# Kernel optimization log

Measured on AMD Instinct MI355X. Metric: run time of the kernel, lower is better.

The kernel has to match this reference:

```python
import jax, jax.numpy as jnp
import numpy as np


def _dconv(x, W, b, d):
    # dilated 3x3 conv, padding=d so spatial size is preserved (NCHW / OIHW)
    y = jax.lax.conv_general_dilated(
        x, W, window_strides=(1, 1), padding=((d, d), (d, d)),
        rhs_dilation=(d, d), dimension_numbers=('NCHW', 'OIHW', 'NCHW'))
    return y + b[None, :, None, None]


def setup_inputs() -> dict:
    key = jax.random.key(0)
    ks = jax.random.split(key, 12)
    B, C, H, W = 2, 512, 64, 64
    s = 0.02  # keep pre-softmax energies in a sane range
    inp = {
        'x':  jax.random.normal(ks[0], (B, C, H, W), jnp.float32),
        'W1': jax.random.normal(ks[1], (128, 512, 3, 3), jnp.float32) * s,
        'b1': jnp.zeros((128,), jnp.float32),
        'W2': jax.random.normal(ks[2], (128, 512, 3, 3), jnp.float32) * s,
        'b2': jnp.zeros((128,), jnp.float32),
        'W3': jax.random.normal(ks[3], (128, 512, 3, 3), jnp.float32) * s,
        'b3': jnp.zeros((128,), jnp.float32),
        'W4': jax.random.normal(ks[4], (128, 512, 3, 3), jnp.float32) * s,
        'b4': jnp.zeros((128,), jnp.float32),
        'Wd':  jax.random.normal(ks[5], (512, 128), jnp.float32) * s,   # dense, 1x1 no bias
        'Wcc': jax.random.normal(ks[6], (256, 512), jnp.float32) * s,   # CCIFL conv 512->256
        'bcc': jnp.zeros((256,), jnp.float32),
        'Wd2': jax.random.normal(ks[7], (512, 256), jnp.float32) * s,   # dense2, 1x1 no bias
    }
    return inp


def reference(x, W1, b1, W2, b2, W3, b3, W4, b4, Wd, Wcc, bcc, Wd2):
    B, C, H, W = x.shape
    N = H * W
    # four dilated-conv feature maps, flattened to [B, 128, N]
    a1 = jax.nn.relu(_dconv(x, W1, b1, 2)).reshape(B, 128, N)
    a2 = jax.nn.relu(_dconv(x, W2, b2, 3)).reshape(B, 128, N)
    a3 = jax.nn.relu(_dconv(x, W3, b3, 5)).reshape(B, 128, N)
    a4 = jax.nn.relu(_dconv(x, W4, b4, 7)).reshape(B, 128, N)

    # spatial attention 1: softmax(a1^T a2), applied as a4 @ att
    att12 = jax.nn.softmax(jnp.einsum('bcn,bcm->bnm', a1, a2), axis=-1)
    o1 = jnp.einsum('bcn,bnm->bcm', a4, att12).reshape(B, 128, H, W)
    o1 = jnp.einsum('oc,bchw->bohw', Wd, o1)  # dense 128->512

    # spatial attention 2: softmax(a3^T a4), applied as a2 @ att
    att34 = jax.nn.softmax(jnp.einsum('bcn,bcm->bnm', a3, a4), axis=-1)
    o2 = jnp.einsum('bcn,bnm->bcm', a2, att34).reshape(B, 128, H, W)
    o2 = jnp.einsum('oc,bchw->bohw', Wd, o2)

    def ccifl(y):
        # GAP -> 1x1 conv (512->256) -> scalar qk attention (softmax over a 1x1 -> 1)
        g = jnp.mean(y, axis=(2, 3))                        # [B, 512]
        z = jnp.einsum('oc,bc->bo', Wcc, g) + bcc           # [B, 256]
        e = jnp.einsum('bc,bc->b', z, z)[:, None, None]     # [B, 1, 1]
        att = jax.nn.softmax(e, axis=-1)                    # == 1
        return z * att[:, 0, :]                             # [B, 256]

    c1 = jnp.einsum('oc,bc->bo', Wd2, ccifl(o1))            # [B, 512]
    c2 = jnp.einsum('oc,bc->bo', Wd2, ccifl(o2))
    # broadcast [B,512,1,1] channel attention over spatial dims + residual
    return c1[:, :, None, None] + c2[:, :, None, None] + x
```

## Files before the change

kernel.cpp:

```cpp
#include <hip/hip_runtime.h>
#include <hip/hip_bf16.h>

typedef short short8 __attribute__((ext_vector_type(8)));
typedef float f32x4 __attribute__((ext_vector_type(4)));
typedef unsigned short u16;

#define XT_OFF   0
#define XT_BYTES (2*78*78*512*2)
#define WR2_OFF  (XT_OFF + XT_BYTES)
#define WR2_BYTES (2*9*16*8*64*16)
#define AFTER_W  (WR2_OFF + WR2_BYTES)
#define P_OFF    AFTER_W
#define P_BYTES  (4*4*4096*128*2)
#define GA_OFF_P (P_OFF + P_BYTES)
#define CA_OFF   AFTER_W
#define CA_BYTES (4*4096*128*4)
#define GA_OFF_A (CA_OFF + CA_BYTES)
#define GA_BYTES 2048
#define GV_REL   GA_BYTES
#define ZV_REL   (GV_REL + 4*512*4)
#define CV_REL   (ZV_REL + 4*256*4)
#define TAIL_END (CV_REL + 2*512*4)
#define WS_NEED_P ((size_t)GA_OFF_P + TAIL_END)
#define WS_NEED_A ((size_t)GA_OFF_A + TAIL_END)

static __device__ __forceinline__ void async_cp16(u16* lds, const u16* g) {
  __builtin_amdgcn_global_load_lds(
      (const __attribute__((address_space(1))) void*)g,
      (__attribute__((address_space(3))) void*)lds, 16, 0, 0);
}

__global__ void zero_u4(uint4* __restrict__ p, int n) {
  int i = blockIdx.x * blockDim.x + threadIdx.x;
  int st = gridDim.x * blockDim.x;
  uint4 z = {0u, 0u, 0u, 0u};
  for (; i < n; i += st) p[i] = z;
}

__global__ void prep_all(const float* __restrict__ x, u16* __restrict__ xT,
                         const float* __restrict__ W2, const float* __restrict__ W4,
                         u16* __restrict__ Wr2, float* __restrict__ gapacc) {
  int bid = blockIdx.x;
  int t = threadIdx.x;
  if (bid < 1024) {
    __shared__ float tile[64][65];
    int bh = bid >> 3, cc = bid & 7;
    int b = bh >> 6, h = bh & 63;
    int w = t & 63, cq4 = t >> 6;
    int pi = t >> 2, q = t & 3;
#pragma unroll
    for (int i = 0; i < 16; ++i) {
      int ci = cq4 + i * 4;
      tile[ci][w] = x[((b * 512 + cc * 64 + ci) * 4096) + h * 64 + w];
    }
    __syncthreads();
    union { u16 u[16]; uint4 v[2]; } pk;
#pragma unroll
    for (int k = 0; k < 16; ++k) {
      __hip_bfloat16 hb = __float2bfloat16(tile[q * 16 + k][pi]);
      pk.u[k] = *(u16*)&hb;
    }
    u16* dst = xT + ((size_t)(b * 78 + h + 7) * 78 + (pi + 7)) * 512 + cc * 64 + q * 16;
    *(uint4*)dst = pk.v[0];
    *(uint4*)(dst + 8) = pk.v[1];
  } else if (bid < 1312) {
    int hb = bid - 1024;
    size_t off; int cnt;
    if (hb < 256) {
      int b = hb >> 7, rem = hb & 127, h = rem >> 1, side = rem & 1;
      off = ((size_t)(b * 78 + 7 + h) * 78 + (side ? 71 : 0)) * 512;
      cnt = 7 * 512;
    } else {
      int k = hb - 256;
      int b = k >> 4, topbot = (k >> 3) & 1, ch = k & 7;
      off = ((size_t)b * 78 + (topbot ? 71 : 0)) * 78 * 512 + (size_t)ch * 34944;
      cnt = 34944;
    }
    uint4* p = (uint4*)(xT + off);
    int n = cnt >> 3;
    uint4 z = {0u, 0u, 0u, 0u};
    for (int i = t; i < n; i += blockDim.x) p[i] = z;
  } else if (bid < 1568) {
    int idx = bid - 1312;
    int conv = idx >> 7, o = idx & 127;
    const float* W = conv ? W4 : W2;
    __shared__ float sw[4608];
    const float* src = W + (size_t)o * 4608;
    for (int k = 0; k < 18; ++k) sw[t + k * 256] = src[t + k * 256];
    __syncthreads();
    if (t < 144) {
      int tap = t >> 4, kc = t & 15;
      int wn = o >> 6, ni = (o >> 4) & 3;
      size_t base = (size_t)conv * 589824 + (size_t)(tap * 16 + kc) * 4096
                    + (wn * 4 + ni) * 512;
#pragma unroll
      for (int cg = 0; cg < 4; ++cg) {
        union { u16 h[8]; uint4 v; } pk;
#pragma unroll
        for (int e = 0; e < 8; ++e) {
          __hip_bfloat16 hb = __float2bfloat16(sw[(kc * 32 + cg * 8 + e) * 9 + tap]);
          pk.h[e] = *(u16*)&hb;
        }
        int lane = cg * 16 + (o & 15);
        *(uint4*)(Wr2 + base + lane * 8) = pk.v;
      }
    }
  } else {
    gapacc[t] = 0.f;
    gapacc[t + 256] = 0.f;
  }
}

template<int MODE>
__global__ __launch_bounds__(256, 2) void conv_mfma(
    const u16* __restrict__ xT, const u16* __restrict__ Wr2,
    u16* __restrict__ Pp, float* __restrict__ convacc) {
  __shared__ __align__(16) u16 Ab[2][8192];
  int bid = blockIdx.x;
  int xcd = bid & 7, j = bid >> 3, g = j >> 2, cq = j & 3;
  int u = g >> 2, pt = (g & 3) * 8 + xcd;
  int b = u & 1, conv = u >> 1;
  int d = conv ? 7 : 3;
  int h0 = pt * 2;
  const u16* xb = xT + (size_t)b * (78 * 78 * 512);
  int t = threadIdx.x, l = t & 63, wv = t >> 6;
  int wm = wv >> 1, wn = wv & 1;

  int slog = (l & 7) ^ (l >> 3);
  int wq = wv * 8 + (l >> 3);
  const u16* gA[4];
#pragma unroll
  for (int m = 0; m < 4; ++m) {
    int hh = m >> 1, mh = m & 1;
    gA[m] = xb + ((size_t)(h0 + hh - d + 7) * 78 + (mh * 32 + wq - d + 7)) * 512
            + cq * 128 + slog * 8;
  }
  const char* bB = (const char*)Wr2 + (size_t)conv * 1179648
                   + cq * 32768 + wn * 4096 + l * 16;

  int rbase = (wm * 64 + (l & 15)) * 64;
  int rs0 = (((l >> 4)) ^ (l & 7)) * 8;
  int rs1 = ((4 + (l >> 4)) ^ (l & 7)) * 8;

  f32x4 acc[4][4];
#pragma unroll
  for (int i = 0; i < 4; ++i)
#pragma unroll
    for (int jj = 0; jj < 4; ++jj) acc[i][jj] = (f32x4){0.f, 0.f, 0.f, 0.f};

  short8 bf0[2][4], bf1[2][4];

  auto issueA = [&](int buf) {
#pragma unroll
    for (int m = 0; m < 4; ++m)
      async_cp16(&Ab[buf][m * 2048 + wv * 512], gA[m]);
    __builtin_amdgcn_sched_barrier(0);
  };
  auto loadB = [&](short8 bf[2][4]) {
#pragma unroll
    for (int c01 = 0; c01 < 2; ++c01)
#pragma unroll
      for (int ni = 0; ni < 4; ++ni)
        bf[c01][ni] = *(const short8*)(bB + c01 * 8192 + ni * 1024);
  };
  auto cbar = [&]() {
    __builtin_amdgcn_sched_barrier(0);
    asm volatile("s_waitcnt vmcnt(8)" ::: "memory");
    __builtin_amdgcn_s_barrier();
    __builtin_amdgcn_sched_barrier(0);
  };
  auto advance = [&](int s) {
    int dA, dB;
    if (!(s & 1)) { dA = 64; dB = 16384; }
    else {
      dB = 114688;
      int tap = (s + 1) >> 1;
      dA = (tap % 3) ? (512 * d - 64) : (38912 * d - 64);
    }
#pragma unroll
    for (int m = 0; m < 4; ++m) gA[m] += dA;
    bB += dB;
  };
  auto compute = [&](int buf, short8 bf[2][4]) {
    const u16* A = Ab[buf];
    short8 af[2][4];
#pragma unroll
    for (int mi = 0; mi < 4; ++mi) {
      af[0][mi] = *(const short8*)&A[rbase + mi * 1024 + rs0];
      af[1][mi] = *(const short8*)&A[rbase + mi * 1024 + rs1];
    }
#pragma unroll
    for (int c01 = 0; c01 < 2; ++c01)
#pragma unroll
      for (int mi = 0; mi < 4; ++mi)
#pragma unroll
        for (int ni = 0; ni < 4; ++ni)
          acc[mi][ni] = __builtin_amdgcn_mfma_f32_16x16x32_bf16(
              af[c01][mi], bf[c01][ni], acc[mi][ni], 0, 0, 0);
  };

  issueA(0); loadB(bf0); advance(0);
  cbar();
  for (int it = 0; it < 9; ++it) {
    int s = it * 2;
    issueA(1); loadB(bf1); advance(s + 1);
    compute(0, bf0);
    cbar();
    if (it < 8) { issueA(0); loadB(bf0); advance(s + 2); }
    compute(1, bf1);
    cbar();
  }

  if (MODE == 0) {
    u16* PP = Pp + ((size_t)(cq * 4 + u) * 4096 + pt * 128 + wm * 64 + (l >> 4) * 4) * 128
              + wn * 64 + (l & 15);
#pragma unroll
    for (int mi = 0; mi < 4; ++mi)
#pragma unroll
      for (int ni = 0; ni < 4; ++ni)
#pragma unroll
        for (int jj = 0; jj < 4; ++jj) {
          __hip_bfloat16 hv = __float2bfloat16(acc[mi][ni][jj]);
          PP[(mi * 16 + jj) * 128 + ni * 16] = *(u16*)&hv;
        }
  } else {
    float* ca = convacc + (size_t)u * 4096 * 128;
#pragma unroll
    for (int mi = 0; mi < 4; ++mi)
#pragma unroll
      for (int ni = 0; ni < 4; ++ni)
#pragma unroll
        for (int jj = 0; jj < 4; ++jj) {
          int pos = pt * 128 + wm * 64 + mi * 16 + (l >> 4) * 4 + jj;
          int oc = wn * 64 + ni * 16 + (l & 15);
          atomicAdd(&ca[pos * 128 + oc], acc[mi][ni][jj]);
        }
  }
}

__global__ void reduce_gap_p(const u16* __restrict__ P,
                             const float* __restrict__ b2, const float* __restrict__ b4,
                             float* __restrict__ gapacc) {
  int u = blockIdx.x >> 6, g = blockIdx.x & 63;
  int conv = u >> 1;
  const float* bias = conv ? b4 : b2;
  int t = threadIdx.x;
  int oct = (t & 15) * 8, pl = t >> 4;
  float bi[8];
  *(float4*)&bi[0] = *(const float4*)&bias[oct];
  *(float4*)&bi[4] = *(const float4*)&bias[oct + 4];
  float s[8];
#pragma unroll
  for (int e = 0; e < 8; ++e) s[e] = 0.f;
  for (int i = 0; i < 4; ++i) {
    int pos = g * 64 + pl * 4 + i;
    size_t base = ((size_t)u * 4096 + pos) * 128 + oct;
    float v[8];
#pragma unroll
    for (int e = 0; e < 8; ++e) v[e] = bi[e];
#pragma unroll
    for (int cq = 0; cq < 4; ++cq) {
      uint4 q = *(const uint4*)&P[base + (size_t)cq * 2097152];
      unsigned w[4] = {q.x, q.y, q.z, q.w};
#pragma unroll
      for (int k = 0; k < 4; ++k) {
        v[k * 2]     += __builtin_bit_cast(float, (w[k] & 0xffffu) << 16);
        v[k * 2 + 1] += __builtin_bit_cast(float, w[k] & 0xffff0000u);
      }
    }
#pragma unroll
    for (int e = 0; e < 8; ++e) s[e] += v[e] > 0.f ? v[e] : 0.f;
  }
  __shared__ float red[16][128];
#pragma unroll
  for (int e = 0; e < 8; ++e) red[pl][oct + e] = s[e];
  __syncthreads();
  if (t < 128) {
    float acc = 0.f;
#pragma unroll
    for (int r = 0; r < 16; ++r) acc += red[r][t];
    atomicAdd(&gapacc[u * 128 + t], acc);
  }
}

__global__ void reduce_gap_a(const float* __restrict__ convacc,
                             const float* __restrict__ b2, const float* __restrict__ b4,
                             float* __restrict__ gapacc) {
  int unit = blockIdx.x >> 5, chunk = blockIdx.x & 31;
  int conv = unit >> 1;
  const float* bias = conv ? b4 : b2;
  int t = threadIdx.x, oc = t & 127, half = t >> 7;
  const float* ca = convacc + (size_t)unit * 4096 * 128;
  float bi = bias[oc];
  float s = 0.f;
  for (int i = 0; i < 64; ++i) {
    int pos = chunk * 128 + half * 64 + i;
    float v = ca[pos * 128 + oc] + bi;
    s += v > 0.f ? v : 0.f;
  }
  __shared__ float red[2][128];
  red[half][oc] = s;
  __syncthreads();
  if (t < 128) atomicAdd(&gapacc[unit * 128 + t], red[0][t] + red[1][t]);
}

__global__ void dense1(const float* __restrict__ gapacc, const float* __restrict__ Wd,
                       float* __restrict__ gv) {
  int o = blockIdx.x, t = threadIdx.x;
  float w = Wd[o * 128 + t];
  float p0 = w * gapacc[2 * 128 + t];
  float p1 = w * gapacc[0 * 128 + t];
  float p2 = w * gapacc[3 * 128 + t];
  float p3 = w * gapacc[1 * 128 + t];
#pragma unroll
  for (int m = 1; m < 64; m <<= 1) {
    p0 += __shfl_xor(p0, m); p1 += __shfl_xor(p1, m);
    p2 += __shfl_xor(p2, m); p3 += __shfl_xor(p3, m);
  }
  __shared__ float red[2][4];
  if ((t & 63) == 0) {
    red[t >> 6][0] = p0; red[t >> 6][1] = p1;
    red[t >> 6][2] = p2; red[t >> 6][3] = p3;
  }
  __syncthreads();
  if (t < 4) {
    const float inv = 1.f / 4096.f;
    gv[t * 512 + o] = (red[0][t] + red[1][t]) * inv;
  }
}

__global__ void dense2(const float* __restrict__ gv, const float* __restrict__ Wcc,
                       const float* __restrict__ bcc, float* __restrict__ zv) {
  int o = blockIdx.x, t = threadIdx.x;
  float w0 = Wcc[o * 512 + t], w1 = Wcc[o * 512 + 256 + t];
  float p[4];
#pragma unroll
  for (int c = 0; c < 4; ++c)
    p[c] = w0 * gv[c * 512 + t] + w1 * gv[c * 512 + 256 + t];
#pragma unroll
  for (int m = 1; m < 64; m <<= 1)
#pragma unroll
    for (int c = 0; c < 4; ++c) p[c] += __shfl_xor(p[c], m);
  __shared__ float red[4][4];
  if ((t & 63) == 0)
#pragma unroll
    for (int c = 0; c < 4; ++c) red[t >> 6][c] = p[c];
  __syncthreads();
  if (t < 4) {
    float s = bcc[o];
#pragma unroll
    for (int wv = 0; wv < 4; ++wv) s += red[wv][t];
    zv[t * 256 + o] = s;
  }
}

__global__ void dense3(const float* __restrict__ zv, const float* __restrict__ Wd2,
                       float* __restrict__ cvec) {
  int o = blockIdx.x, t = threadIdx.x;
  float w = Wd2[o * 256 + t];
  float p0 = w * (zv[0 * 256 + t] + zv[1 * 256 + t]);
  float p1 = w * (zv[2 * 256 + t] + zv[3 * 256 + t]);
#pragma unroll
  for (int m = 1; m < 64; m <<= 1) {
    p0 += __shfl_xor(p0, m);
    p1 += __shfl_xor(p1, m);
  }
  __shared__ float red[4][2];
  if ((t & 63) == 0) { red[t >> 6][0] = p0; red[t >> 6][1] = p1; }
  __syncthreads();
  if (t < 2) {
    float s = red[0][t] + red[1][t] + red[2][t] + red[3][t];
    cvec[t * 512 + o] = s;
  }
}

__global__ void final_add(const float* __restrict__ x, const float* __restrict__ cvec,
                          float* __restrict__ out) {
  int i = blockIdx.x * blockDim.x + threadIdx.x;
  int st = gridDim.x * blockDim.x;
  const float4* x4 = (const float4*)x;
  float4* o4 = (float4*)out;
  for (; i < 1048576; i += st) {
    int flat = i << 2;
    int b = flat >> 21;
    int ch = (flat >> 12) & 511;
    float c = cvec[b * 512 + ch];
    float4 v = x4[i];
    v.x += c; v.y += c; v.z += c; v.w += c;
    o4[i] = v;
  }
}

extern "C" void kernel_launch(void* const* d_in, const int* in_sizes, int n_in,
                              void* d_out, int out_size, void* d_ws, size_t ws_size,
                              hipStream_t stream) {
  const float* x   = (const float*)d_in[0];
  const float* W2  = (const float*)d_in[3];
  const float* b2  = (const float*)d_in[4];
  const float* W4  = (const float*)d_in[7];
  const float* b4  = (const float*)d_in[8];
  const float* Wd  = (const float*)d_in[9];
  const float* Wcc = (const float*)d_in[10];
  const float* bcc = (const float*)d_in[11];
  const float* Wd2 = (const float*)d_in[12];
  float* out = (float*)d_out;

  char* ws = (char*)d_ws;
  u16* xT  = (u16*)(ws + XT_OFF);
  u16* Wr2 = (u16*)(ws + WR2_OFF);

  const bool partial = ws_size >= WS_NEED_P;
  size_t ga_off = partial ? GA_OFF_P : GA_OFF_A;
  float* gapacc = (float*)(ws + ga_off);
  float* gv     = (float*)(ws + ga_off + GV_REL);
  float* zv     = (float*)(ws + ga_off + ZV_REL);
  float* cvec   = (float*)(ws + ga_off + CV_REL);

  prep_all<<<1569, 256, 0, stream>>>(x, xT, W2, W4, Wr2, gapacc);

  if (partial) {
    u16* Pp = (u16*)(ws + P_OFF);
    conv_mfma<0><<<512, 256, 0, stream>>>(xT, Wr2, Pp, nullptr);
    reduce_gap_p<<<256, 256, 0, stream>>>(Pp, b2, b4, gapacc);
  } else {
    float* convacc = (float*)(ws + CA_OFF);
    zero_u4<<<512, 256, 0, stream>>>((uint4*)convacc, CA_BYTES / 16);
    conv_mfma<1><<<512, 256, 0, stream>>>(xT, Wr2, nullptr, convacc);
    reduce_gap_a<<<128, 256, 0, stream>>>(convacc, b2, b4, gapacc);
  }

  dense1<<<512, 128, 0, stream>>>(gapacc, Wd, gv);
  dense2<<<256, 256, 0, stream>>>(gv, Wcc, bcc, zv);
  dense3<<<512, 256, 0, stream>>>(zv, Wd2, cvec);
  final_add<<<2048, 256, 0, stream>>>(x, cvec, out);
}
```

Before: 56.42 us.

## Fold Wcc·Wd into fused weight, merge dense tail into final add, retile conv waves

Precomputes a fused Wcc·Wd matrix inside the prep kernel so the GAP-to-z path needs one small GEMV instead of two. The Wd2 matvec is folded into final_add, with each block recomputing its channel scalar, which removes two kernel launches. The conv MFMA kernel's wave tiling changes from a 2x2 split to each wave covering all 128 rows and 32 output channels, with fewer B registers and a tighter vmcnt wait. In exchange, final_add blocks repeat a 256-wide dot product and the conv waves read more A fragments from LDS.

```diff
diff --git a/kernel.cpp b/kernel.cpp
--- a/kernel.cpp
+++ b/kernel.cpp
@@ -17,10 +17,9 @@
 #define CA_BYTES (4*4096*128*4)
 #define GA_OFF_A (CA_OFF + CA_BYTES)
 #define GA_BYTES 2048
-#define GV_REL   GA_BYTES
-#define ZV_REL   (GV_REL + 4*512*4)
-#define CV_REL   (ZV_REL + 4*256*4)
-#define TAIL_END (CV_REL + 2*512*4)
+#define ZV_REL   GA_BYTES
+#define WF_REL   (ZV_REL + 4*256*4)
+#define TAIL_END (WF_REL + 256*128*4)
 #define WS_NEED_P ((size_t)GA_OFF_P + TAIL_END)
 #define WS_NEED_A ((size_t)GA_OFF_A + TAIL_END)
 
@@ -39,12 +38,32 @@
 
 __global__ void prep_all(const float* __restrict__ x, u16* __restrict__ xT,
                          const float* __restrict__ W2, const float* __restrict__ W4,
-                         u16* __restrict__ Wr2, float* __restrict__ gapacc) {
+                         const float* __restrict__ Wd, const float* __restrict__ Wcc,
+                         u16* __restrict__ Wr2, float* __restrict__ Wfuse,
+                         float* __restrict__ gapacc) {
+  __shared__ float smem[4608];
   int bid = blockIdx.x;
   int t = threadIdx.x;
-  if (bid < 1024) {
-    __shared__ float tile[64][65];
-    int bh = bid >> 3, cc = bid & 7;
+  if (bid < 256) {
+    int o2 = bid;
+    float* wcc_s = smem;
+    float* part  = smem + 512;
+    wcc_s[t] = Wcc[o2 * 512 + t];
+    wcc_s[t + 256] = Wcc[o2 * 512 + 256 + t];
+    __syncthreads();
+    int c = t & 127, half = t >> 7;
+    float s = 0.f;
+    int o0 = half * 256;
+#pragma unroll 4
+    for (int o = 0; o < 256; ++o)
+      s += wcc_s[o0 + o] * Wd[(o0 + o) * 128 + c];
+    if (half) part[c] = s;
+    __syncthreads();
+    if (!half) Wfuse[o2 * 128 + c] = s + part[c];
+  } else if (bid < 1280) {
+    float (*tile)[65] = (float(*)[65])smem;
+    int pb = bid - 256;
+    int bh = pb >> 3, cc = pb & 7;
     int b = bh >> 6, h = bh & 63;
     int w = t & 63, cq4 = t >> 6;
     int pi = t >> 2, q = t & 3;
@@ -63,8 +82,8 @@
     u16* dst = xT + ((size_t)(b * 78 + h + 7) * 78 + (pi + 7)) * 512 + cc * 64 + q * 16;
     *(uint4*)dst = pk.v[0];
     *(uint4*)(dst + 8) = pk.v[1];
-  } else if (bid < 1312) {
-    int hb = bid - 1024;
+  } else if (bid < 1568) {
+    int hb = bid - 1280;
     size_t off; int cnt;
     if (hb < 256) {
       int b = hb >> 7, rem = hb & 127, h = rem >> 1, side = rem & 1;
@@ -80,11 +99,11 @@
     int n = cnt >> 3;
     uint4 z = {0u, 0u, 0u, 0u};
     for (int i = t; i < n; i += blockDim.x) p[i] = z;
-  } else if (bid < 1568) {
-    int idx = bid - 1312;
+  } else if (bid < 1824) {
+    int idx = bid - 1568;
     int conv = idx >> 7, o = idx & 127;
     const float* W = conv ? W4 : W2;
-    __shared__ float sw[4608];
+    float* sw = smem;
     const float* src = W + (size_t)o * 4608;
     for (int k = 0; k < 18; ++k) sw[t + k * 256] = src[t + k * 256];
     __syncthreads();
@@ -124,7 +143,6 @@
   int h0 = pt * 2;
   const u16* xb = xT + (size_t)b * (78 * 78 * 512);
   int t = threadIdx.x, l = t & 63, wv = t >> 6;
-  int wm = wv >> 1, wn = wv & 1;
 
   int slog = (l & 7) ^ (l >> 3);
   int wq = wv * 8 + (l >> 3);
@@ -136,19 +154,19 @@
             + cq * 128 + slog * 8;
   }
   const char* bB = (const char*)Wr2 + (size_t)conv * 1179648
-                   + cq * 32768 + wn * 4096 + l * 16;
-
-  int rbase = (wm * 64 + (l & 15)) * 64;
+                   + cq * 32768 + wv * 2048 + l * 16;
+
+  int rbase = (l & 15) * 64;
   int rs0 = (((l >> 4)) ^ (l & 7)) * 8;
   int rs1 = ((4 + (l >> 4)) ^ (l & 7)) * 8;
 
-  f32x4 acc[4][4];
-#pragma unroll
-  for (int i = 0; i < 4; ++i)
-#pragma unroll
-    for (int jj = 0; jj < 4; ++jj) acc[i][jj] = (f32x4){0.f, 0.f, 0.f, 0.f};
-
-  short8 bf0[2][4], bf1[2][4];
+  f32x4 acc[8][2];
+#pragma unroll
+  for (int i = 0; i < 8; ++i)
+#pragma unroll
+    for (int jj = 0; jj < 2; ++jj) acc[i][jj] = (f32x4){0.f, 0.f, 0.f, 0.f};
+
+  short8 bf0[2][2], bf1[2][2];
 
   auto issueA = [&](int buf) {
 #pragma unroll
@@ -156,16 +174,16 @@
       async_cp16(&Ab[buf][m * 2048 + wv * 512], gA[m]);
     __builtin_amdgcn_sched_barrier(0);
   };
-  auto loadB = [&](short8 bf[2][4]) {
+  auto loadB = [&](short8 bf[2][2]) {
 #pragma unroll
     for (int c01 = 0; c01 < 2; ++c01)
 #pragma unroll
-      for (int ni = 0; ni < 4; ++ni)
+      for (int ni = 0; ni < 2; ++ni)
         bf[c01][ni] = *(const short8*)(bB + c01 * 8192 + ni * 1024);
   };
   auto cbar = [&]() {
     __builtin_amdgcn_sched_barrier(0);
-    asm volatile("s_waitcnt vmcnt(8)" ::: "memory");
+    asm volatile("s_waitcnt vmcnt(4)" ::: "memory");
     __builtin_amdgcn_s_barrier();
     __builtin_amdgcn_sched_barrier(0);
   };
@@ -181,22 +199,17 @@
     for (int m = 0; m < 4; ++m) gA[m] += dA;
     bB += dB;
   };
-  auto compute = [&](int buf, short8 bf[2][4]) {
+  auto compute = [&](int buf, short8 bf[2][2]) {
     const u16* A = Ab[buf];
-    short8 af[2][4];
-#pragma unroll
-    for (int mi = 0; mi < 4; ++mi) {
-      af[0][mi] = *(const short8*)&A[rbase + mi * 1024 + rs0];
-      af[1][mi] = *(const short8*)&A[rbase + mi * 1024 + rs1];
-    }
-#pragma unroll
-    for (int c01 = 0; c01 < 2; ++c01)
-#pragma unroll
-      for (int mi = 0; mi < 4; ++mi)
-#pragma unroll
-        for (int ni = 0; ni < 4; ++ni)
-          acc[mi][ni] = __builtin_amdgcn_mfma_f32_16x16x32_bf16(
-              af[c01][mi], bf[c01][ni], acc[mi][ni], 0, 0, 0);
+#pragma unroll
+    for (int mi = 0; mi < 8; ++mi) {
+      short8 a0 = *(const short8*)&A[rbase + mi * 1024 + rs0];
+      short8 a1 = *(const short8*)&A[rbase + mi * 1024 + rs1];
+      acc[mi][0] = __builtin_amdgcn_mfma_f32_16x16x32_bf16(a0, bf[0][0], acc[mi][0], 0, 0, 0);
+      acc[mi][1] = __builtin_amdgcn_mfma_f32_16x16x32_bf16(a0, bf[0][1], acc[mi][1], 0, 0, 0);
+      acc[mi][0] = __builtin_amdgcn_mfma_f32_16x16x32_bf16(a1, bf[1][0], acc[mi][0], 0, 0, 0);
+      acc[mi][1] = __builtin_amdgcn_mfma_f32_16x16x32_bf16(a1, bf[1][1], acc[mi][1], 0, 0, 0);
+    }
   };
 
   issueA(0); loadB(bf0); advance(0);
@@ -212,12 +225,12 @@
   }
 
   if (MODE == 0) {
-    u16* PP = Pp + ((size_t)(cq * 4 + u) * 4096 + pt * 128 + wm * 64 + (l >> 4) * 4) * 128
-              + wn * 64 + (l & 15);
-#pragma unroll
-    for (int mi = 0; mi < 4; ++mi)
-#pragma unroll
-      for (int ni = 0; ni < 4; ++ni)
+    u16* PP = Pp + ((size_t)(cq * 4 + u) * 4096 + pt * 128 + (l >> 4) * 4) * 128
+              + wv * 32 + (l & 15);
+#pragma unroll
+    for (int mi = 0; mi < 8; ++mi)
+#pragma unroll
+      for (int ni = 0; ni < 2; ++ni)
 #pragma unroll
         for (int jj = 0; jj < 4; ++jj) {
           __hip_bfloat16 hv = __float2bfloat16(acc[mi][ni][jj]);
@@ -226,13 +239,13 @@
   } else {
     float* ca = convacc + (size_t)u * 4096 * 128;
 #pragma unroll
-    for (int mi = 0; mi < 4; ++mi)
-#pragma unroll
-      for (int ni = 0; ni < 4; ++ni)
+    for (int mi = 0; mi < 8; ++mi)
+#pragma unroll
+      for (int ni = 0; ni < 2; ++ni)
 #pragma unroll
         for (int jj = 0; jj < 4; ++jj) {
-          int pos = pt * 128 + wm * 64 + mi * 16 + (l >> 4) * 4 + jj;
-          int oc = wn * 64 + ni * 16 + (l & 15);
+          int pos = pt * 128 + mi * 16 + (l >> 4) * 4 + jj;
+          int oc = wv * 32 + ni * 16 + (l & 15);
           atomicAdd(&ca[pos * 128 + oc], acc[mi][ni][jj]);
         }
   }
@@ -304,10 +317,10 @@
   if (t < 128) atomicAdd(&gapacc[unit * 128 + t], red[0][t] + red[1][t]);
 }
 
-__global__ void dense1(const float* __restrict__ gapacc, const float* __restrict__ Wd,
-                       float* __restrict__ gv) {
-  int o = blockIdx.x, t = threadIdx.x;
-  float w = Wd[o * 128 + t];
+__global__ void dense_a(const float* __restrict__ gapacc, const float* __restrict__ Wfuse,
+                        const float* __restrict__ bcc, float* __restrict__ zv) {
+  int o2 = blockIdx.x, t = threadIdx.x;
+  float w = Wfuse[o2 * 128 + t];
   float p0 = w * gapacc[2 * 128 + t];
   float p1 = w * gapacc[0 * 128 + t];
   float p2 = w * gapacc[3 * 128 + t];
@@ -325,70 +338,39 @@
   __syncthreads();
   if (t < 4) {
     const float inv = 1.f / 4096.f;
-    gv[t * 512 + o] = (red[0][t] + red[1][t]) * inv;
-  }
-}
-
-__global__ void dense2(const float* __restrict__ gv, const float* __restrict__ Wcc,
-                       const float* __restrict__ bcc, float* __restrict__ zv) {
-  int o = blockIdx.x, t = threadIdx.x;
-  float w0 = Wcc[o * 512 + t], w1 = Wcc[o * 512 + 256 + t];
-  float p[4];
-#pragma unroll
-  for (int c = 0; c < 4; ++c)
-    p[c] = w0 * gv[c * 512 + t] + w1 * gv[c * 512 + 256 + t];
-#pragma unroll
-  for (int m = 1; m < 64; m <<= 1)
-#pragma unroll
-    for (int c = 0; c < 4; ++c) p[c] += __shfl_xor(p[c], m);
-  __shared__ float red[4][4];
-  if ((t & 63) == 0)
-#pragma unroll
-    for (int c = 0; c < 4; ++c) red[t >> 6][c] = p[c];
-  __syncthreads();
-  if (t < 4) {
-    float s = bcc[o];
-#pragma unroll
-    for (int wv = 0; wv < 4; ++wv) s += red[wv][t];
-    zv[t * 256 + o] = s;
-  }
-}
-
-__global__ void dense3(const float* __restrict__ zv, const float* __restrict__ Wd2,
-                       float* __restrict__ cvec) {
-  int o = blockIdx.x, t = threadIdx.x;
-  float w = Wd2[o * 256 + t];
-  float p0 = w * (zv[0 * 256 + t] + zv[1 * 256 + t]);
-  float p1 = w * (zv[2 * 256 + t] + zv[3 * 256 + t]);
+    zv[t * 256 + o2] = bcc[o2] + (red[0][t] + red[1][t]) * inv;
+  }
+}
+
+__global__ void final_add(const float* __restrict__ x, const float* __restrict__ zv,
+                          const float* __restrict__ Wd2, float* __restrict__ out) {
+  int t = threadIdx.x, bid = blockIdx.x;
+  int ch = (bid >> 2) & 511;
+  float w = Wd2[ch * 256 + t];
+  float p0 = w * (zv[t] + zv[256 + t]);
+  float p1 = w * (zv[512 + t] + zv[768 + t]);
 #pragma unroll
   for (int m = 1; m < 64; m <<= 1) {
     p0 += __shfl_xor(p0, m);
     p1 += __shfl_xor(p1, m);
   }
   __shared__ float red[4][2];
+  __shared__ float cv[2];
   if ((t & 63) == 0) { red[t >> 6][0] = p0; red[t >> 6][1] = p1; }
   __syncthreads();
-  if (t < 2) {
-    float s = red[0][t] + red[1][t] + red[2][t] + red[3][t];
-    cvec[t * 512 + o] = s;
-  }
-}
-
-__global__ void final_add(const float* __restrict__ x, const float* __restrict__ cvec,
-                          float* __restrict__ out) {
-  int i = blockIdx.x * blockDim.x + threadIdx.x;
-  int st = gridDim.x * blockDim.x;
+  if (t < 2) cv[t] = red[0][t] + red[1][t] + red[2][t] + red[3][t];
+  __syncthreads();
   const float4* x4 = (const float4*)x;
   float4* o4 = (float4*)out;
-  for (; i < 1048576; i += st) {
-    int flat = i << 2;
-    int b = flat >> 21;
-    int ch = (flat >> 12) & 511;
-    float c = cvec[b * 512 + ch];
-    float4 v = x4[i];
-    v.x += c; v.y += c; v.z += c; v.w += c;
-    o4[i] = v;
-  }
+  int i = bid * 256 + t;
+  float c0 = cv[0], c1 = cv[1];
+  float4 v = x4[i];
+  v.x += c0; v.y += c0; v.z += c0; v.w += c0;
+  o4[i] = v;
+  i += 524288;
+  float4 v2 = x4[i];
+  v2.x += c1; v2.y += c1; v2.z += c1; v2.w += c1;
+  o4[i] = v2;
 }
 
 extern "C" void kernel_launch(void* const* d_in, const int* in_sizes, int n_in,
@@ -412,11 +394,10 @@
   const bool partial = ws_size >= WS_NEED_P;
   size_t ga_off = partial ? GA_OFF_P : GA_OFF_A;
   float* gapacc = (float*)(ws + ga_off);
-  float* gv     = (float*)(ws + ga_off + GV_REL);
   float* zv     = (float*)(ws + ga_off + ZV_REL);
-  float* cvec   = (float*)(ws + ga_off + CV_REL);
-
-  prep_all<<<1569, 256, 0, stream>>>(x, xT, W2, W4, Wr2, gapacc);
+  float* wfuse  = (float*)(ws + ga_off + WF_REL);
+
+  prep_all<<<1825, 256, 0, stream>>>(x, xT, W2, W4, Wd, Wcc, Wr2, wfuse, gapacc);
 
   if (partial) {
     u16* Pp = (u16*)(ws + P_OFF);
@@ -429,8 +410,6 @@
     reduce_gap_a<<<128, 256, 0, stream>>>(convacc, b2, b4, gapacc);
   }
 
-  dense1<<<512, 128, 0, stream>>>(gapacc, Wd, gv);
-  dense2<<<256, 256, 0, stream>>>(gv, Wcc, bcc, zv);
-  dense3<<<512, 256, 0, stream>>>(zv, Wd2, cvec);
-  final_add<<<2048, 256, 0, stream>>>(x, cvec, out);
-}
+  dense_a<<<256, 128, 0, stream>>>(gapacc, wfuse, bcc, zv);
+  final_add<<<2048, 256, 0, stream>>>(x, zv, Wd2, out);
+}
```

Result: slower. 66.11 us (+17.2%).
